# Optimization experiments

Measured on AMD Instinct MI355X. Metric: run time of the kernel, lower is better.

The kernel has to match this reference:

```python
import jax, jax.numpy as jnp
import numpy as np

B, N, D_IN, D_OUT = 2, 4096, 768, 768


def setup_inputs() -> dict:
    key = jax.random.key(0)
    kx, kq, kk, kv = jax.random.split(key, 4)
    x = jax.random.normal(kx, (B, N, D_IN), dtype=jnp.float32)
    # Linear(d_in, d_out, bias=False) weights, stored as [d_in, d_out]
    scale = 1.0 / np.sqrt(D_IN)
    Wq = jax.random.normal(kq, (D_IN, D_OUT), dtype=jnp.float32) * scale
    Wk = jax.random.normal(kk, (D_IN, D_OUT), dtype=jnp.float32) * scale
    Wv = jax.random.normal(kv, (D_IN, D_OUT), dtype=jnp.float32) * scale
    return {"x": x, "Wq": Wq, "Wk": Wk, "Wv": Wv}


def reference(x, Wq, Wk, Wv):
    # q,k,v: [B, N, D_OUT]
    q = jnp.einsum('bnd,de->bne', x, Wq)
    k = jnp.einsum('bnd,de->bne', x, Wk)
    v = jnp.einsum('bnd,de->bne', x, Wv)
    # Full [B, N, N] score matrix (naive attention, as in source).
    # NOTE: source's masked_fill is non-in-place and discarded, so NO causal
    # mask is actually applied -- reproduced faithfully here.
    scores = jnp.einsum('bqe,bke->bqk', q, k) / jnp.sqrt(jnp.float32(k.shape[-1]))
    weights = jax.nn.softmax(scores, axis=-1)
    # dropout rate 0.0 / eval mode -> identity
    out = jnp.einsum('bqk,bke->bqe', weights, v)  # [B, N, D_OUT]
    return out
```

## Files before the change

kernel.cpp:

```cpp
#include <hip/hip_runtime.h>

typedef __bf16 bf16x8 __attribute__((ext_vector_type(8)));
typedef float f32x4 __attribute__((ext_vector_type(4)));
typedef unsigned short us8 __attribute__((ext_vector_type(8)));

#define GAS __attribute__((address_space(1)))
#define LAS __attribute__((address_space(3)))

__device__ __forceinline__ unsigned short f32_to_bf16(float f) {
    unsigned int u = __float_as_uint(f);
    u += 0x7FFFu + ((u >> 16) & 1u);
    return (unsigned short)(u >> 16);
}

__device__ __forceinline__ float bf16_to_f32(unsigned short h) {
    return __uint_as_float((unsigned int)h << 16);
}

__device__ __forceinline__ void load16(const unsigned short* g, unsigned short* l) {
    __builtin_amdgcn_global_load_lds((GAS unsigned int*)g, (LAS unsigned int*)l, 16, 0, 0);
}

__global__ __launch_bounds__(1024) void prep(
    const float* __restrict__ x, unsigned short* __restrict__ Xbf,
    const float* __restrict__ W0, const float* __restrict__ W1, const float* __restrict__ W2,
    unsigned short* __restrict__ T0, unsigned short* __restrict__ T1, unsigned short* __restrict__ T2,
    float* __restrict__ lsum)
{
    __shared__ float tile[32][33];
    const int id = blockIdx.x;
    const int t = threadIdx.x;
    if (id < 1536) {
        int i = id * 1024 + t;
        float4 v = ((const float4*)x)[i];
        ushort4 o;
        o.x = f32_to_bf16(v.x); o.y = f32_to_bf16(v.y);
        o.z = f32_to_bf16(v.z); o.w = f32_to_bf16(v.w);
        ((ushort4*)Xbf)[i] = o;
    } else if (id < 3264) {
        const int tid = id - 1536;
        const int z = tid / 576, rem = tid % 576;
        const int by = rem / 24, bx = rem % 24;
        const float* W = (z == 0) ? W0 : (z == 1) ? W1 : W2;
        unsigned short* T = (z == 0) ? T0 : (z == 1) ? T1 : T2;
        const int r0 = by * 32, c0 = bx * 32;
        const int tx = t & 31, ty = t >> 5;
        tile[ty][tx] = W[(size_t)(r0 + ty) * 768 + c0 + tx];
        __syncthreads();
        T[(size_t)(c0 + ty) * 768 + r0 + tx] = f32_to_bf16(tile[tx][ty]);
    } else {
        float4 z4 = {0.f, 0.f, 0.f, 0.f};
        ((float4*)lsum)[t] = z4;
        ((float4*)lsum)[t + 1024] = z4;
    }
}

__global__ __launch_bounds__(256) void qkv_proj(
    const unsigned short* __restrict__ Xbf,
    const unsigned short* __restrict__ Wt,
    unsigned short* __restrict__ QK,
    unsigned short* __restrict__ Vt)
{
    const int id = blockIdx.x;
    const unsigned short* A; const unsigned short* B;
    unsigned short* C; int ldc, m0, n0;
    if (id < 768) {
        const int z = id / 384, r = id % 384;
        A = Xbf; B = Wt + (size_t)z * 589824; C = QK + (size_t)z * 6291456;
        ldc = 768;
        m0 = (r / 6) * 128; n0 = (r % 6) * 128;
    } else {
        const int j = id - 768;
        A = Wt + 1179648ull;
        B = Xbf; C = Vt;
        ldc = 8192;
        m0 = (j >> 6) * 128; n0 = (j & 63) * 128;
    }
    const int lda = 768, ldb = 768;
    const int t = threadIdx.x;
    const int lane = t & 63;
    const int w = t >> 6;
    const int wm = (w >> 1) * 64;
    const int wn = (w & 1) * 64;

    __shared__ unsigned short At[128 * 64];
    __shared__ unsigned short Bt[128 * 64];

    f32x4 acc[4][4];
#pragma unroll
    for (int i = 0; i < 4; ++i)
#pragma unroll
        for (int j2 = 0; j2 < 4; ++j2) acc[i][j2] = (f32x4){0.f, 0.f, 0.f, 0.f};

    const int r15 = lane & 15;
    const int qa = lane >> 4;

    for (int k0 = 0; k0 < 768; k0 += 64) {
#pragma unroll
        for (int i = 0; i < 4; ++i) {
            const int c = i * 256 + t;
            const int row = c >> 3;
            const int cc = (c & 7) ^ (row & 7);
            load16(A + (size_t)(m0 + row) * lda + k0 + cc * 8, &At[c * 8]);
            load16(B + (size_t)(n0 + row) * ldb + k0 + cc * 8, &Bt[c * 8]);
        }
        __syncthreads();

#pragma unroll
        for (int ks = 0; ks < 2; ++ks) {
            bf16x8 af[4], bf[4];
#pragma unroll
            for (int mi = 0; mi < 4; ++mi) {
                const int row = wm + mi * 16 + r15;
                af[mi] = *(const bf16x8*)&At[row * 64 + (((ks << 2) + qa) ^ (row & 7)) * 8];
            }
#pragma unroll
            for (int ni = 0; ni < 4; ++ni) {
                const int row = wn + ni * 16 + r15;
                bf[ni] = *(const bf16x8*)&Bt[row * 64 + (((ks << 2) + qa) ^ (row & 7)) * 8];
            }
#pragma unroll
            for (int mi = 0; mi < 4; ++mi)
#pragma unroll
                for (int ni = 0; ni < 4; ++ni)
                    acc[mi][ni] = __builtin_amdgcn_mfma_f32_16x16x32_bf16(
                        af[mi], bf[ni], acc[mi][ni], 0, 0, 0);
        }
        __syncthreads();
    }

    const int cr = (lane >> 4) * 4;
#pragma unroll
    for (int mi = 0; mi < 4; ++mi)
#pragma unroll
        for (int ni = 0; ni < 4; ++ni) {
            const int gm = m0 + wm + mi * 16 + cr;
            const int gn = n0 + wn + ni * 16 + r15;
#pragma unroll
            for (int r = 0; r < 4; ++r)
                C[(size_t)(gm + r) * ldc + gn] = f32_to_bf16(acc[mi][ni][r]);
        }
}

__global__ __launch_bounds__(512, 2) void gemm_s_exp2(
    const unsigned short* __restrict__ Q, const unsigned short* __restrict__ Kb,
    unsigned short* __restrict__ Sexp, float* __restrict__ lsum, float alpha)
{
    const int f = blockIdx.x;
    const int xcd = f & 7;
    const int local = f >> 3;
    const int x = (xcd & 1) * 8 + (local & 7);
    const int y = ((xcd >> 1) & 1) * 8 + (local >> 3);
    const int bb = xcd >> 2;
    const unsigned short* A = Q + (size_t)bb * 3145728;
    const unsigned short* B = Kb + (size_t)bb * 3145728;
    unsigned short* C = Sexp + (size_t)bb * 16777216;
    float* ls = lsum + bb * 4096;
    const int m0 = y * 256, n0 = x * 256;
    const int lda = 768, ldb = 768, ldc = 4096;
    constexpr int NT = 12;

    __shared__ unsigned short As[2][256 * 64];
    __shared__ unsigned short Bs[2][256 * 64];

    const int t = threadIdx.x;
    const int lane = t & 63;
    const int w = t >> 6;
    const int wm = (w >> 2) * 128;
    const int wn = (w & 3) * 64;
    const int r15 = lane & 15;
    const int qa = lane >> 4;

    const unsigned short* srcA[4];
    const unsigned short* srcB[4];
    int dst[4];
#pragma unroll
    for (int i = 0; i < 4; ++i) {
        const int c = i * 512 + t;
        const int row = c >> 3;
        const int cc = (c & 7) ^ (row & 7);
        srcA[i] = A + (size_t)(m0 + row) * lda + cc * 8;
        srcB[i] = B + (size_t)(n0 + row) * ldb + cc * 8;
        dst[i] = c * 8;
    }

    auto stage = [&](int buf, int kbase) {
#pragma unroll
        for (int i = 0; i < 4; ++i)
            load16(srcA[i] + kbase, &As[buf][dst[i]]);
#pragma unroll
        for (int i = 0; i < 4; ++i)
            load16(srcB[i] + kbase, &Bs[buf][dst[i]]);
    };

    int offA[8][2], offB[4][2];
#pragma unroll
    for (int mi = 0; mi < 8; ++mi) {
        const int row = wm + mi * 16 + r15;
#pragma unroll
        for (int ks = 0; ks < 2; ++ks)
            offA[mi][ks] = row * 64 + (((ks << 2) + qa) ^ (row & 7)) * 8;
    }
#pragma unroll
    for (int ni = 0; ni < 4; ++ni) {
        const int row = wn + ni * 16 + r15;
#pragma unroll
        for (int ks = 0; ks < 2; ++ks)
            offB[ni][ks] = row * 64 + (((ks << 2) + qa) ^ (row & 7)) * 8;
    }

    f32x4 acc[8][4];
#pragma unroll
    for (int i = 0; i < 8; ++i)
#pragma unroll
        for (int j = 0; j < 4; ++j) acc[i][j] = (f32x4){0.f, 0.f, 0.f, 0.f};

    stage(0, 0);
    stage(1, 64);

    for (int tt = 0; tt < NT; ++tt) {
        const int b = tt & 1;
        if (tt == NT - 1) {
            asm volatile("s_waitcnt vmcnt(0)" ::: "memory");
        } else {
            asm volatile("s_waitcnt vmcnt(8)" ::: "memory");
        }
        __builtin_amdgcn_s_barrier();

#pragma unroll
        for (int ks = 0; ks < 2; ++ks) {
            bf16x8 aA[8], bB[4];
#pragma unroll
            for (int i = 0; i < 8; ++i)
                aA[i] = *(const bf16x8*)&As[b][offA[i][ks]];
#pragma unroll
            for (int ni = 0; ni < 4; ++ni)
                bB[ni] = *(const bf16x8*)&Bs[b][offB[ni][ks]];
#pragma unroll
            for (int i = 0; i < 8; ++i)
#pragma unroll
                for (int ni = 0; ni < 4; ++ni)
                    acc[i][ni] = __builtin_amdgcn_mfma_f32_16x16x32_bf16(
                        aA[i], bB[ni], acc[i][ni], 0, 0, 0);
        }

        asm volatile("" ::: "memory");
        __builtin_amdgcn_s_barrier();

        if (tt + 2 < NT) stage(b, (tt + 2) << 6);
    }

    const int cr = (lane >> 4) * 4;
#pragma unroll
    for (int mi = 0; mi < 8; ++mi) {
        const int gm = m0 + wm + mi * 16 + cr;
        float rs0 = 0.f, rs1 = 0.f, rs2 = 0.f, rs3 = 0.f;
#pragma unroll
        for (int ni = 0; ni < 4; ++ni) {
            const int gn = n0 + wn + ni * 16 + r15;
            float v0 = __expf(alpha * acc[mi][ni][0]);
            float v1 = __expf(alpha * acc[mi][ni][1]);
            float v2 = __expf(alpha * acc[mi][ni][2]);
            float v3 = __expf(alpha * acc[mi][ni][3]);
            C[(size_t)(gm + 0) * ldc + gn] = f32_to_bf16(v0);
            C[(size_t)(gm + 1) * ldc + gn] = f32_to_bf16(v1);
            C[(size_t)(gm + 2) * ldc + gn] = f32_to_bf16(v2);
            C[(size_t)(gm + 3) * ldc + gn] = f32_to_bf16(v3);
            rs0 += v0; rs1 += v1; rs2 += v2; rs3 += v3;
        }
#pragma unroll
        for (int m = 1; m < 16; m <<= 1) {
            rs0 += __shfl_xor(rs0, m, 64);
            rs1 += __shfl_xor(rs1, m, 64);
            rs2 += __shfl_xor(rs2, m, 64);
            rs3 += __shfl_xor(rs3, m, 64);
        }
        if (r15 == 0) {
            atomicAdd(&ls[gm + 0], rs0);
            atomicAdd(&ls[gm + 1], rs1);
            atomicAdd(&ls[gm + 2], rs2);
            atomicAdd(&ls[gm + 3], rs3);
        }
    }
}

__global__ __launch_bounds__(512, 2) void gemm_out(
    const unsigned short* __restrict__ P, const unsigned short* __restrict__ Vt,
    const float* __restrict__ lsum, float* __restrict__ out)
{
    const int f = blockIdx.x;
    const int xcd = f & 7;
    const int batch = xcd >> 2;
    const int nb = xcd & 3;
    const int mb = f >> 3;
    const unsigned short* A = P + (size_t)batch * 16777216;
    const unsigned short* B = Vt + (size_t)batch * 4096;
    const float* ls = lsum + batch * 4096;
    float* C = out + (size_t)batch * 3145728;
    const int m0 = mb * 128, n0 = nb * 192;
    const int lda = 4096, ldb = 8192;
    constexpr int NT = 64;

    __shared__ unsigned short As[3][128 * 64];
    __shared__ unsigned short Bs[3][192 * 64];

    const int t = threadIdx.x;
    const int lane = t & 63;
    const int w = t >> 6;
    const int wm = (w >> 2) * 64;
    const int wn = (w & 3) * 48;
    const int r15 = lane & 15;
    const int qa = lane >> 4;

    const unsigned short* srcA[2];
    int dstA[2];
#pragma unroll
    for (int i = 0; i < 2; ++i) {
        const int c = i * 512 + t;
        const int row = c >> 3;
        const int cc = (c & 7) ^ (row & 7);
        srcA[i] = A + (size_t)(m0 + row) * lda + cc * 8;
        dstA[i] = c * 8;
    }
    const unsigned short* srcB[3];
    int dstB[3];
#pragma unroll
    for (int i = 0; i < 3; ++i) {
        const int c = i * 512 + t;
        const int row = c >> 3;
        const int cc = (c & 7) ^ (row & 7);
        srcB[i] = B + (size_t)(n0 + row) * ldb + cc * 8;
        dstB[i] = c * 8;
    }

    auto stage = [&](int buf, int kbase) {
#pragma unroll
        for (int i = 0; i < 2; ++i)
            load16(srcA[i] + kbase, &As[buf][dstA[i]]);
#pragma unroll
        for (int i = 0; i < 3; ++i)
            load16(srcB[i] + kbase, &Bs[buf][dstB[i]]);
    };

    int offA[4][2], offB[3][2];
#pragma unroll
    for (int mi = 0; mi < 4; ++mi) {
        const int row = wm + mi * 16 + r15;
#pragma unroll
        for (int ks = 0; ks < 2; ++ks)
            offA[mi][ks] = row * 64 + (((ks << 2) + qa) ^ (row & 7)) * 8;
    }
#pragma unroll
    for (int ni = 0; ni < 3; ++ni) {
        const int row = wn + ni * 16 + r15;
#pragma unroll
        for (int ks = 0; ks < 2; ++ks)
            offB[ni][ks] = row * 64 + (((ks << 2) + qa) ^ (row & 7)) * 8;
    }

    f32x4 acc[4][3];
#pragma unroll
    for (int i = 0; i < 4; ++i)
#pragma unroll
        for (int j = 0; j < 3; ++j) acc[i][j] = (f32x4){0.f, 0.f, 0.f, 0.f};

    stage(0, 0);
    stage(1, 64);
    stage(2, 128);

    int b = 0;
    for (int tt = 0; tt < NT; ++tt) {
        if (tt < NT - 2) {
            asm volatile("s_waitcnt vmcnt(10)" ::: "memory");
        } else if (tt == NT - 2) {
            asm volatile("s_waitcnt vmcnt(5)" ::: "memory");
        } else {
            asm volatile("s_waitcnt vmcnt(0)" ::: "memory");
        }
        __builtin_amdgcn_s_barrier();

#pragma unroll
        for (int ks = 0; ks < 2; ++ks) {
            bf16x8 aA[4], bB[3];
#pragma unroll
            for (int i = 0; i < 4; ++i)
                aA[i] = *(const bf16x8*)&As[b][offA[i][ks]];
#pragma unroll
            for (int ni = 0; ni < 3; ++ni)
                bB[ni] = *(const bf16x8*)&Bs[b][offB[ni][ks]];
#pragma unroll
            for (int i = 0; i < 4; ++i)
#pragma unroll
                for (int ni = 0; ni < 3; ++ni)
                    acc[i][ni] = __builtin_amdgcn_mfma_f32_16x16x32_bf16(
                        aA[i], bB[ni], acc[i][ni], 0, 0, 0);
        }

        asm volatile("" ::: "memory");
        __builtin_amdgcn_s_barrier();

        if (tt + 3 < NT) stage(b, (tt + 3) << 6);
        b = (b == 2) ? 0 : b + 1;
    }

    const int cr = (lane >> 4) * 4;
#pragma unroll
    for (int mi = 0; mi < 4; ++mi) {
        const int gm = m0 + wm + mi * 16 + cr;
        const float i0 = 1.f / ls[gm + 0];
        const float i1 = 1.f / ls[gm + 1];
        const float i2 = 1.f / ls[gm + 2];
        const float i3 = 1.f / ls[gm + 3];
#pragma unroll
        for (int ni = 0; ni < 3; ++ni) {
            const int gn = n0 + wn + ni * 16 + r15;
            C[(size_t)(gm + 0) * 768 + gn] = acc[mi][ni][0] * i0;
            C[(size_t)(gm + 1) * 768 + gn] = acc[mi][ni][1] * i1;
            C[(size_t)(gm + 2) * 768 + gn] = acc[mi][ni][2] * i2;
            C[(size_t)(gm + 3) * 768 + gn] = acc[mi][ni][3] * i3;
        }
    }
}

extern "C" void kernel_launch(void* const* d_in, const int* in_sizes, int n_in,
                              void* d_out, int out_size, void* d_ws, size_t ws_size,
                              hipStream_t stream) {
    const float* x  = (const float*)d_in[0];
    const float* Wq = (const float*)d_in[1];
    const float* Wk = (const float*)d_in[2];
    const float* Wv = (const float*)d_in[3];
    float* out = (float*)d_out;

    char* base = (char*)d_ws;
    size_t off = 0;
    auto alloc = [&](size_t b) { char* p = base + off; off += (b + 255) & ~(size_t)255; return p; };

    unsigned short* Xbf = (unsigned short*)alloc(8192ull * 768 * 2);
    unsigned short* WqT = (unsigned short*)alloc(768ull * 768 * 2);
    unsigned short* WkT = (unsigned short*)alloc(768ull * 768 * 2);
    unsigned short* WvT = (unsigned short*)alloc(768ull * 768 * 2);
    unsigned short* Qb  = (unsigned short*)alloc(8192ull * 768 * 2);
    unsigned short* Kb  = (unsigned short*)alloc(8192ull * 768 * 2);
    unsigned short* Vt  = (unsigned short*)alloc(768ull * 8192 * 2);
    unsigned short* Sexp = (unsigned short*)alloc(2ull * 4096 * 4096 * 2);
    float* lsum = (float*)alloc(2ull * 4096 * 4);
    (void)ws_size; (void)in_sizes; (void)n_in; (void)out_size; (void)WkT; (void)WvT;

    prep<<<dim3(3265), dim3(1024), 0, stream>>>(x, Xbf, Wq, Wk, Wv, WqT, WkT, WvT, lsum);
    qkv_proj<<<dim3(1152), dim3(256), 0, stream>>>(Xbf, WqT, Qb, Vt);
    gemm_s_exp2<<<dim3(512), dim3(512), 0, stream>>>(
        Qb, Kb, Sexp, lsum, 0.03608439182435161f);
    gemm_out<<<dim3(256), dim3(512), 0, stream>>>(Sexp, Vt, lsum, out);
}
```

Baseline: 271.9 us.

## Split QKV projection into double-buffered large-tile Q/K and V^T GEMM kernels

Replaces the single 128x128-tile QKV projection with two kernels. One computes Q and K together with 256x192 tiles; the other computes V^T with 192x128 tiles. Both use double-buffered async global-to-LDS loads with explicit vmcnt waits and XCD-aware block mapping. This aims to improve data reuse and overlap loads with MFMA. It also drops the 2-blocks-per-CU launch bound on the attention GEMMs and remaps gemm_out blocks across XCDs for locality. The trade-offs are higher register and LDS use per block and an extra kernel launch.

```diff
diff --git a/kernel.cpp b/kernel.cpp
--- a/kernel.cpp
+++ b/kernel.cpp
@@ -55,85 +55,254 @@
     }
 }
 
-__global__ __launch_bounds__(256) void qkv_proj(
+__global__ __launch_bounds__(512) void qk2(
     const unsigned short* __restrict__ Xbf,
-    const unsigned short* __restrict__ Wt,
-    unsigned short* __restrict__ QK,
-    unsigned short* __restrict__ Vt)
+    const unsigned short* __restrict__ Wqk,
+    unsigned short* __restrict__ Qb,
+    unsigned short* __restrict__ Kb)
 {
-    const int id = blockIdx.x;
-    const unsigned short* A; const unsigned short* B;
-    unsigned short* C; int ldc, m0, n0;
-    if (id < 768) {
-        const int z = id / 384, r = id % 384;
-        A = Xbf; B = Wt + (size_t)z * 589824; C = QK + (size_t)z * 6291456;
-        ldc = 768;
-        m0 = (r / 6) * 128; n0 = (r % 6) * 128;
-    } else {
-        const int j = id - 768;
-        A = Wt + 1179648ull;
-        B = Xbf; C = Vt;
-        ldc = 8192;
-        m0 = (j >> 6) * 128; n0 = (j & 63) * 128;
-    }
-    const int lda = 768, ldb = 768;
+    const int f = blockIdx.x;
+    const int xcd = f & 7;
+    const int local = f >> 3;
+    const int mb = xcd * 4 + (local >> 3);
+    const int nb = local & 7;
+    const unsigned short* A = Xbf;
+    const unsigned short* B = Wqk;
+    unsigned short* C = (nb < 4) ? Qb : Kb;
+    const int m0 = mb * 256;
+    const int n0 = nb * 192;
+    const int c0 = (nb & 3) * 192;
+    const int lda = 768, ldb = 768, ldc = 768;
+    constexpr int NT = 12;
+
+    __shared__ unsigned short As[2][256 * 64];
+    __shared__ unsigned short Bs[2][192 * 64];
+
     const int t = threadIdx.x;
     const int lane = t & 63;
     const int w = t >> 6;
-    const int wm = (w >> 1) * 64;
-    const int wn = (w & 1) * 64;
-
-    __shared__ unsigned short At[128 * 64];
-    __shared__ unsigned short Bt[128 * 64];
-
-    f32x4 acc[4][4];
-#pragma unroll
-    for (int i = 0; i < 4; ++i)
-#pragma unroll
-        for (int j2 = 0; j2 < 4; ++j2) acc[i][j2] = (f32x4){0.f, 0.f, 0.f, 0.f};
-
+    const int wm = (w >> 2) * 128;
+    const int wn = (w & 3) * 48;
     const int r15 = lane & 15;
     const int qa = lane >> 4;
 
-    for (int k0 = 0; k0 < 768; k0 += 64) {
-#pragma unroll
-        for (int i = 0; i < 4; ++i) {
-            const int c = i * 256 + t;
-            const int row = c >> 3;
-            const int cc = (c & 7) ^ (row & 7);
-            load16(A + (size_t)(m0 + row) * lda + k0 + cc * 8, &At[c * 8]);
-            load16(B + (size_t)(n0 + row) * ldb + k0 + cc * 8, &Bt[c * 8]);
-        }
-        __syncthreads();
+    const unsigned short* srcA[4];
+    int dstA[4];
+#pragma unroll
+    for (int i = 0; i < 4; ++i) {
+        const int c = i * 512 + t;
+        const int row = c >> 3;
+        const int cc = (c & 7) ^ (row & 7);
+        srcA[i] = A + (size_t)(m0 + row) * lda + cc * 8;
+        dstA[i] = c * 8;
+    }
+    const unsigned short* srcB[3];
+    int dstB[3];
+#pragma unroll
+    for (int i = 0; i < 3; ++i) {
+        const int c = i * 512 + t;
+        const int row = c >> 3;
+        const int cc = (c & 7) ^ (row & 7);
+        srcB[i] = B + (size_t)(n0 + row) * ldb + cc * 8;
+        dstB[i] = c * 8;
+    }
+
+    auto stage = [&](int buf, int kbase) {
+#pragma unroll
+        for (int i = 0; i < 4; ++i) load16(srcA[i] + kbase, &As[buf][dstA[i]]);
+#pragma unroll
+        for (int i = 0; i < 3; ++i) load16(srcB[i] + kbase, &Bs[buf][dstB[i]]);
+    };
+
+    int offA[8][2], offB[3][2];
+#pragma unroll
+    for (int mi = 0; mi < 8; ++mi) {
+        const int row = wm + mi * 16 + r15;
+#pragma unroll
+        for (int ks = 0; ks < 2; ++ks)
+            offA[mi][ks] = row * 64 + (((ks << 2) + qa) ^ (row & 7)) * 8;
+    }
+#pragma unroll
+    for (int ni = 0; ni < 3; ++ni) {
+        const int row = wn + ni * 16 + r15;
+#pragma unroll
+        for (int ks = 0; ks < 2; ++ks)
+            offB[ni][ks] = row * 64 + (((ks << 2) + qa) ^ (row & 7)) * 8;
+    }
+
+    f32x4 acc[8][3];
+#pragma unroll
+    for (int i = 0; i < 8; ++i)
+#pragma unroll
+        for (int j = 0; j < 3; ++j) acc[i][j] = (f32x4){0.f, 0.f, 0.f, 0.f};
+
+    stage(0, 0);
+    stage(1, 64);
+
+    for (int tt = 0; tt < NT; ++tt) {
+        const int b = tt & 1;
+        if (tt == NT - 1) {
+            asm volatile("s_waitcnt vmcnt(0)" ::: "memory");
+        } else {
+            asm volatile("s_waitcnt vmcnt(7)" ::: "memory");
+        }
+        __builtin_amdgcn_s_barrier();
 
 #pragma unroll
         for (int ks = 0; ks < 2; ++ks) {
-            bf16x8 af[4], bf[4];
-#pragma unroll
-            for (int mi = 0; mi < 4; ++mi) {
-                const int row = wm + mi * 16 + r15;
-                af[mi] = *(const bf16x8*)&At[row * 64 + (((ks << 2) + qa) ^ (row & 7)) * 8];
-            }
-#pragma unroll
-            for (int ni = 0; ni < 4; ++ni) {
-                const int row = wn + ni * 16 + r15;
-                bf[ni] = *(const bf16x8*)&Bt[row * 64 + (((ks << 2) + qa) ^ (row & 7)) * 8];
-            }
-#pragma unroll
-            for (int mi = 0; mi < 4; ++mi)
-#pragma unroll
-                for (int ni = 0; ni < 4; ++ni)
-                    acc[mi][ni] = __builtin_amdgcn_mfma_f32_16x16x32_bf16(
-                        af[mi], bf[ni], acc[mi][ni], 0, 0, 0);
-        }
-        __syncthreads();
+            bf16x8 aA[8], bB[3];
+#pragma unroll
+            for (int i = 0; i < 8; ++i)
+                aA[i] = *(const bf16x8*)&As[b][offA[i][ks]];
+#pragma unroll
+            for (int ni = 0; ni < 3; ++ni)
+                bB[ni] = *(const bf16x8*)&Bs[b][offB[ni][ks]];
+#pragma unroll
+            for (int i = 0; i < 8; ++i)
+#pragma unroll
+                for (int ni = 0; ni < 3; ++ni)
+                    acc[i][ni] = __builtin_amdgcn_mfma_f32_16x16x32_bf16(
+                        aA[i], bB[ni], acc[i][ni], 0, 0, 0);
+        }
+
+        asm volatile("" ::: "memory");
+        __builtin_amdgcn_s_barrier();
+
+        if (tt + 2 < NT) stage(b, (tt + 2) << 6);
     }
 
     const int cr = (lane >> 4) * 4;
 #pragma unroll
-    for (int mi = 0; mi < 4; ++mi)
-#pragma unroll
-        for (int ni = 0; ni < 4; ++ni) {
+    for (int mi = 0; mi < 8; ++mi)
+#pragma unroll
+        for (int ni = 0; ni < 3; ++ni) {
+            const int gm = m0 + wm + mi * 16 + cr;
+            const int gn = c0 + wn + ni * 16 + r15;
+#pragma unroll
+            for (int r = 0; r < 4; ++r)
+                C[(size_t)(gm + r) * ldc + gn] = f32_to_bf16(acc[mi][ni][r]);
+        }
+}
+
+__global__ __launch_bounds__(512) void vt2(
+    const unsigned short* __restrict__ WvT,
+    const unsigned short* __restrict__ Xbf,
+    unsigned short* __restrict__ Vt)
+{
+    const int f = blockIdx.x;
+    const int xcd = f & 7;
+    const int local = f >> 3;
+    const int nb = xcd * 8 + (local >> 2);
+    const int mb = local & 3;
+    const unsigned short* A = WvT;
+    const unsigned short* B = Xbf;
+    unsigned short* C = Vt;
+    const int m0 = mb * 192;
+    const int n0 = nb * 128;
+    const int lda = 768, ldb = 768, ldc = 8192;
+    constexpr int NT = 12;
+
+    __shared__ unsigned short As[2][192 * 64];
+    __shared__ unsigned short Bs[2][128 * 64];
+
+    const int t = threadIdx.x;
+    const int lane = t & 63;
+    const int w = t >> 6;
+    const int wm = (w >> 2) * 96;
+    const int wn = (w & 3) * 32;
+    const int r15 = lane & 15;
+    const int qa = lane >> 4;
+
+    const unsigned short* srcA[3];
+    int dstA[3];
+#pragma unroll
+    for (int i = 0; i < 3; ++i) {
+        const int c = i * 512 + t;
+        const int row = c >> 3;
+        const int cc = (c & 7) ^ (row & 7);
+        srcA[i] = A + (size_t)(m0 + row) * lda + cc * 8;
+        dstA[i] = c * 8;
+    }
+    const unsigned short* srcB[2];
+    int dstB[2];
+#pragma unroll
+    for (int i = 0; i < 2; ++i) {
+        const int c = i * 512 + t;
+        const int row = c >> 3;
+        const int cc = (c & 7) ^ (row & 7);
+        srcB[i] = B + (size_t)(n0 + row) * ldb + cc * 8;
+        dstB[i] = c * 8;
+    }
+
+    auto stage = [&](int buf, int kbase) {
+#pragma unroll
+        for (int i = 0; i < 3; ++i) load16(srcA[i] + kbase, &As[buf][dstA[i]]);
+#pragma unroll
+        for (int i = 0; i < 2; ++i) load16(srcB[i] + kbase, &Bs[buf][dstB[i]]);
+    };
+
+    int offA[6][2], offB[2][2];
+#pragma unroll
+    for (int mi = 0; mi < 6; ++mi) {
+        const int row = wm + mi * 16 + r15;
+#pragma unroll
+        for (int ks = 0; ks < 2; ++ks)
+            offA[mi][ks] = row * 64 + (((ks << 2) + qa) ^ (row & 7)) * 8;
+    }
+#pragma unroll
+    for (int ni = 0; ni < 2; ++ni) {
+        const int row = wn + ni * 16 + r15;
+#pragma unroll
+        for (int ks = 0; ks < 2; ++ks)
+            offB[ni][ks] = row * 64 + (((ks << 2) + qa) ^ (row & 7)) * 8;
+    }
+
+    f32x4 acc[6][2];
+#pragma unroll
+    for (int i = 0; i < 6; ++i)
+#pragma unroll
+        for (int j = 0; j < 2; ++j) acc[i][j] = (f32x4){0.f, 0.f, 0.f, 0.f};
+
+    stage(0, 0);
+    stage(1, 64);
+
+    for (int tt = 0; tt < NT; ++tt) {
+        const int b = tt & 1;
+        if (tt == NT - 1) {
+            asm volatile("s_waitcnt vmcnt(0)" ::: "memory");
+        } else {
+            asm volatile("s_waitcnt vmcnt(5)" ::: "memory");
+        }
+        __builtin_amdgcn_s_barrier();
+
+#pragma unroll
+        for (int ks = 0; ks < 2; ++ks) {
+            bf16x8 aA[6], bB[2];
+#pragma unroll
+            for (int i = 0; i < 6; ++i)
+                aA[i] = *(const bf16x8*)&As[b][offA[i][ks]];
+#pragma unroll
+            for (int ni = 0; ni < 2; ++ni)
+                bB[ni] = *(const bf16x8*)&Bs[b][offB[ni][ks]];
+#pragma unroll
+            for (int i = 0; i < 6; ++i)
+#pragma unroll
+                for (int ni = 0; ni < 2; ++ni)
+                    acc[i][ni] = __builtin_amdgcn_mfma_f32_16x16x32_bf16(
+                        aA[i], bB[ni], acc[i][ni], 0, 0, 0);
+        }
+
+        asm volatile("" ::: "memory");
+        __builtin_amdgcn_s_barrier();
+
+        if (tt + 2 < NT) stage(b, (tt + 2) << 6);
+    }
+
+    const int cr = (lane >> 4) * 4;
+#pragma unroll
+    for (int mi = 0; mi < 6; ++mi)
+#pragma unroll
+        for (int ni = 0; ni < 2; ++ni) {
             const int gm = m0 + wm + mi * 16 + cr;
             const int gn = n0 + wn + ni * 16 + r15;
 #pragma unroll
@@ -142,7 +311,7 @@
         }
 }
 
-__global__ __launch_bounds__(512, 2) void gemm_s_exp2(
+__global__ __launch_bounds__(512) void gemm_s_exp2(
     const unsigned short* __restrict__ Q, const unsigned short* __restrict__ Kb,
     unsigned short* __restrict__ Sexp, float* __restrict__ lsum, float alpha)
 {
@@ -284,15 +453,17 @@
     }
 }
 
-__global__ __launch_bounds__(512, 2) void gemm_out(
+__global__ __launch_bounds__(512) void gemm_out(
     const unsigned short* __restrict__ P, const unsigned short* __restrict__ Vt,
     const float* __restrict__ lsum, float* __restrict__ out)
 {
     const int f = blockIdx.x;
     const int xcd = f & 7;
-    const int batch = xcd >> 2;
-    const int nb = xcd & 3;
-    const int mb = f >> 3;
+    const int local = f >> 3;
+    const int nb = local & 3;
+    const int rg = xcd * 8 + (local >> 2);
+    const int batch = rg >> 5;
+    const int mb = rg & 31;
     const unsigned short* A = P + (size_t)batch * 16777216;
     const unsigned short* B = Vt + (size_t)batch * 4096;
     const float* ls = lsum + batch * 4096;
@@ -447,7 +618,8 @@
     (void)ws_size; (void)in_sizes; (void)n_in; (void)out_size; (void)WkT; (void)WvT;
 
     prep<<<dim3(3265), dim3(1024), 0, stream>>>(x, Xbf, Wq, Wk, Wv, WqT, WkT, WvT, lsum);
-    qkv_proj<<<dim3(1152), dim3(256), 0, stream>>>(Xbf, WqT, Qb, Vt);
+    qk2<<<dim3(256), dim3(512), 0, stream>>>(Xbf, WqT, Qb, Kb);
+    vt2<<<dim3(256), dim3(512), 0, stream>>>(WvT, Xbf, Vt);
     gemm_s_exp2<<<dim3(512), dim3(512), 0, stream>>>(
         Qb, Kb, Sexp, lsum, 0.03608439182435161f);
     gemm_out<<<dim3(256), dim3(512), 0, stream>>>(Sexp, Vt, lsum, out);
```

Measured after the change: 257.8 us. 1.05x faster.
